# Optimization experiments

Hardware: AMD Instinct MI355X
Metric: run time of the kernel (lower is better)

Reference implementation:

```python
import jax, jax.numpy as jnp
import numpy as np

BETA = 1.0  # init kwarg beta
TAU = 0.5   # init kwarg tau


def setup_inputs() -> dict:
    key = jax.random.key(0)
    k1, k2, k3, k4, k5 = jax.random.split(key, 5)
    M, N, D = 6, 2048, 1152  # views, batch, flattened feature dim (Linear(1152,128))
    return {
        "x_all": jax.random.normal(k1, (M, N, D), jnp.float32),
        "W": jax.random.normal(k2, (D, 128), jnp.float32) * 0.03,  # line_layers weight (in,out)
        "b": jax.random.normal(k3, (128,), jnp.float32) * 0.01,    # line_layers bias
        "U": jax.random.normal(k4, (128, 64), jnp.float32),
        "V": jax.random.normal(k5, (128, 64), jnp.float32),
    }


def _retrieve(x, P):
    # x: [M, N, 128], P: [128, 64]
    # per-sample: P @ softmax(beta * (P.T @ x_i))  ==  softmax(beta * x @ P) @ P.T  (batched)
    attn = jax.nn.softmax(BETA * jnp.einsum('mnd,dk->mnk', x, P), axis=-1)  # [M,N,64]
    return jnp.einsum('mnk,dk->mnd', attn, P)  # [M,N,128]


def _pair_loss_sum(E):
    # E: [M, N, 128]. Sum of losses over all ordered pairs of distinct views.
    M, N = E.shape[0], E.shape[1]
    sim = jnp.einsum('mnd,kpd->mknp', E, E) / TAU          # [M,M,N,N]
    pos = jnp.diagonal(sim, axis1=2, axis2=3)              # [M,M,N] positives (diag)
    # negatives = off-diagonal entries of each row; exclude diag via -inf for stable logsumexp
    neg = jnp.where(jnp.eye(N, dtype=bool), -jnp.inf, sim)
    lse = jax.nn.logsumexp(neg, axis=-1)                   # [M,M,N]
    # -log(exp(pos)/sum(exp(neg))) == lse - pos
    per_pair = (lse - pos).mean(axis=-1)                   # [M,M]
    off_diag = 1.0 - jnp.eye(M, dtype=per_pair.dtype)      # skip i == j (torch.equal check)
    return (per_pair * off_diag).sum()


def reference(x_all, W, b, U, V):
    M, N = x_all.shape[0], x_all.shape[1]
    x = x_all.reshape(M, N, -1) @ W + b                    # Linear(1152, 128)
    Ue = _retrieve(x, U)
    Ve = _retrieve(x, V)
    total = _pair_loss_sum(Ue) + _pair_loss_sum(Ve)
    return total / (2 * M * (M - 1))
```

## Files before the change

kernel.cpp:

```cpp
#include <hip/hip_runtime.h>
#include <hip/hip_bf16.h>

#define M_VIEWS 6
#define N_ROWS  2048
#define D_IN    1152
#define D_HID   128
#define D_K     64
#define TOT_ROWS (M_VIEWS * N_ROWS)
#define SCALE_E 1.6986436f
#define LOG2E   1.4426950408889634f

typedef short bf16x8 __attribute__((ext_vector_type(8)));
typedef float f32x4  __attribute__((ext_vector_type(4)));

typedef __attribute__((address_space(1))) const void gvoid_t;
typedef __attribute__((address_space(3))) void svoid_t;

__device__ inline void async16(const void* g, void* l) {
    __builtin_amdgcn_global_load_lds((gvoid_t*)g, (svoid_t*)l, 16, 0, 0);
}

#if __has_builtin(__builtin_amdgcn_exp2f)
__device__ inline float fexp2(float x) { return __builtin_amdgcn_exp2f(x); }
#else
__device__ inline float fexp2(float x) { return exp2f(x); }
#endif
#if __has_builtin(__builtin_amdgcn_logf)
__device__ inline float flog2(float x) { return __builtin_amdgcn_logf(x); }
#else
__device__ inline float flog2(float x) { return log2f(x); }
#endif

__device__ inline short2 splitf(float v) {
    __hip_bfloat16 hb = __float2bfloat16(v);
    float rem = v - __bfloat162float(hb);
    __hip_bfloat16 lb = __float2bfloat16(rem);
    short2 r;
    r.x = *reinterpret_cast<const short*>(&hb);
    r.y = *reinterpret_cast<const short*>(&lb);
    return r;
}

__device__ inline short bf16of(float v) {
    __hip_bfloat16 hb = __float2bfloat16(v);
    return *reinterpret_cast<const short*>(&hb);
}

__global__ __launch_bounds__(64) void prep_w_kernel(
    const float* __restrict__ W, __hip_bfloat16* __restrict__ Whi)
{
    const int s    = blockIdx.x >> 3;
    const int ct   = blockIdx.x & 7;
    const int lane = threadIdx.x;
    const int lg = lane >> 4, lr = lane & 15;
    bf16x8 hi;
    #pragma unroll
    for (int i = 0; i < 8; ++i)
        hi[i] = bf16of(W[(size_t)(s * 32 + lg * 8 + i) * D_HID + ct * 16 + lr]);
    size_t off = ((size_t)(s * 8 + ct) * 64 + lane) * 8;
    *reinterpret_cast<bf16x8*>(Whi + off) = hi;
}

__global__ __launch_bounds__(64) void prep_p_kernel(
    const float* __restrict__ U, const float* __restrict__ V,
    __hip_bfloat16* __restrict__ Pfhi, __hip_bfloat16* __restrict__ Pflo)
{
    const int blk = blockIdx.x;
    const int mat = blk >> 5, f = blk & 31;
    const float* P = mat ? V : U;
    const int lane = threadIdx.x, lg = lane >> 4, lr = lane & 15;
    bf16x8 hi, lo;
    #pragma unroll
    for (int i = 0; i < 8; ++i) {
        float w;
        if (f < 16) {
            int s = f >> 2, ct = f & 3;
            w = P[(size_t)(s * 32 + lg * 8 + i) * D_K + ct * 16 + lr] * LOG2E;
        } else {
            int g = f - 16, s2 = g >> 3, ct2 = g & 7;
            w = P[(size_t)(ct2 * 16 + lr) * D_K + s2 * 32 + lg * 8 + i];
        }
        short2 hl = splitf(w);
        hi[i] = hl.x; lo[i] = hl.y;
    }
    size_t off = ((size_t)(mat * 32 + f) * 64 + lane) * 8;
    *reinterpret_cast<bf16x8*>(Pfhi + off) = hi;
    *reinterpret_cast<bf16x8*>(Pflo + off) = lo;
}

__global__ __launch_bounds__(256) void xretrieve_kernel(
    const float* __restrict__ xall,
    const __hip_bfloat16* __restrict__ Whi,
    const float* __restrict__ bias,
    const __hip_bfloat16* __restrict__ Pfhi,
    const __hip_bfloat16* __restrict__ Pflo,
    __hip_bfloat16* __restrict__ E)
{
    __shared__ __align__(16) char smem[24576];
    f32x4* red = reinterpret_cast<f32x4*>(smem);
    float* xs  = reinterpret_cast<float*>(smem);
    float* alb = reinterpret_cast<float*>(smem + 8448);

    const int wave = threadIdx.x >> 6, lane = threadIdx.x & 63;
    const int lg = lane >> 4, lr = lane & 15;
    const int row0 = blockIdx.x * 16;

    const float* ap = xall + (size_t)(row0 + lr) * D_IN + wave * 288;
    f32x4 acc[8];
    #pragma unroll
    for (int ct = 0; ct < 8; ++ct) acc[ct] = {0.f, 0.f, 0.f, 0.f};

    const bf16x8* whb = reinterpret_cast<const bf16x8*>(Whi) + lane;
    for (int s = 0; s < 9; ++s) {
        const int gs = wave * 9 + s;
        const float* a8 = ap + s * 32 + lg * 8;
        float4 va = *reinterpret_cast<const float4*>(a8);
        float4 vb = *reinterpret_cast<const float4*>(a8 + 4);
        bf16x8 ah;
        ah[0] = bf16of(va.x); ah[1] = bf16of(va.y);
        ah[2] = bf16of(va.z); ah[3] = bf16of(va.w);
        ah[4] = bf16of(vb.x); ah[5] = bf16of(vb.y);
        ah[6] = bf16of(vb.z); ah[7] = bf16of(vb.w);
        #pragma unroll
        for (int ct = 0; ct < 8; ++ct) {
            bf16x8 wh = whb[(size_t)(gs * 8 + ct) * 64];
            acc[ct] = __builtin_amdgcn_mfma_f32_16x16x32_bf16(ah, wh, acc[ct], 0, 0, 0);
        }
    }

    if (wave > 0) {
        #pragma unroll
        for (int ct = 0; ct < 8; ++ct)
            red[(wave - 1) * 512 + ct * 64 + lane] = acc[ct];
    }
    __syncthreads();
    if (wave == 0) {
        f32x4 xv[8];
        #pragma unroll
        for (int ct = 0; ct < 8; ++ct) {
            f32x4 a = acc[ct];
            a += red[ct * 64 + lane];
            a += red[512 + ct * 64 + lane];
            a += red[1024 + ct * 64 + lane];
            float bj = bias[ct * 16 + lr];
            #pragma unroll
            for (int j = 0; j < 4; ++j) xv[ct][j] = a[j] + bj;
        }
        __syncthreads();
        #pragma unroll
        for (int ct = 0; ct < 8; ++ct)
            #pragma unroll
            for (int j = 0; j < 4; ++j)
                xs[(lg * 4 + j) * 132 + ct * 16 + lr] = xv[ct][j];
    } else {
        __syncthreads();
    }
    __syncthreads();

    const int mat = wave;
    if (wave < 2) {
        bf16x8 xh[4], xl[4];
        #pragma unroll
        for (int s = 0; s < 4; ++s) {
            const float* xp = xs + lr * 132 + s * 32 + lg * 8;
            float4 va = *reinterpret_cast<const float4*>(xp);
            float4 vb = *reinterpret_cast<const float4*>(xp + 4);
            float v[8] = {va.x, va.y, va.z, va.w, vb.x, vb.y, vb.z, vb.w};
            #pragma unroll
            for (int i = 0; i < 8; ++i) {
                short2 hl = splitf(v[i]);
                xh[s][i] = hl.x; xl[s][i] = hl.y;
            }
        }

        const bf16x8* bh = reinterpret_cast<const bf16x8*>(Pfhi) + (size_t)mat * 32 * 64 + lane;
        const bf16x8* bl = reinterpret_cast<const bf16x8*>(Pflo) + (size_t)mat * 32 * 64 + lane;

        f32x4 lacc[4];
        #pragma unroll
        for (int ct = 0; ct < 4; ++ct) lacc[ct] = {0.f, 0.f, 0.f, 0.f};
        #pragma unroll
        for (int ct = 0; ct < 4; ++ct) {
            #pragma unroll
            for (int s = 0; s < 4; ++s) {
                bf16x8 wh = bh[(s * 4 + ct) * 64];
                bf16x8 wl = bl[(s * 4 + ct) * 64];
                lacc[ct] = __builtin_amdgcn_mfma_f32_16x16x32_bf16(xh[s], wh, lacc[ct], 0, 0, 0);
                lacc[ct] = __builtin_amdgcn_mfma_f32_16x16x32_bf16(xl[s], wh, lacc[ct], 0, 0, 0);
                lacc[ct] = __builtin_amdgcn_mfma_f32_16x16x32_bf16(xh[s], wl, lacc[ct], 0, 0, 0);
            }
        }

        float* al = alb + mat * (16 * 72);
        #pragma unroll
        for (int j = 0; j < 4; ++j) {
            float l0 = lacc[0][j], l1 = lacc[1][j], l2 = lacc[2][j], l3 = lacc[3][j];
            float mx = fmaxf(fmaxf(l0, l1), fmaxf(l2, l3));
            #pragma unroll
            for (int s = 1; s < 16; s <<= 1) mx = fmaxf(mx, __shfl_xor(mx, s));
            float p0 = fexp2(l0 - mx), p1 = fexp2(l1 - mx);
            float p2 = fexp2(l2 - mx), p3 = fexp2(l3 - mx);
            float sm = p0 + p1 + p2 + p3;
            #pragma unroll
            for (int s = 1; s < 16; s <<= 1) sm += __shfl_xor(sm, s);
            float inv = 1.0f / sm;
            float* ar = al + (lg * 4 + j) * 72;
            ar[lr]      = p0 * inv;
            ar[16 + lr] = p1 * inv;
            ar[32 + lr] = p2 * inv;
            ar[48 + lr] = p3 * inv;
        }
    }
    __syncthreads();

    if (wave < 2) {
        const float* al = alb + mat * (16 * 72);
        const bf16x8* bh = reinterpret_cast<const bf16x8*>(Pfhi) + (size_t)mat * 32 * 64 + lane;
        const bf16x8* bl = reinterpret_cast<const bf16x8*>(Pflo) + (size_t)mat * 32 * 64 + lane;

        bf16x8 aah[2], aal[2];
        #pragma unroll
        for (int s2 = 0; s2 < 2; ++s2) {
            const float* ap2 = al + lr * 72 + s2 * 32 + lg * 8;
            float4 va = *reinterpret_cast<const float4*>(ap2);
            float4 vb = *reinterpret_cast<const float4*>(ap2 + 4);
            float v[8] = {va.x, va.y, va.z, va.w, vb.x, vb.y, vb.z, vb.w};
            #pragma unroll
            for (int i = 0; i < 8; ++i) {
                short2 hl = splitf(v[i]);
                aah[s2][i] = hl.x; aal[s2][i] = hl.y;
            }
        }

        f32x4 eacc[8];
        #pragma unroll
        for (int ct2 = 0; ct2 < 8; ++ct2) eacc[ct2] = {0.f, 0.f, 0.f, 0.f};
        #pragma unroll
        for (int ct2 = 0; ct2 < 8; ++ct2) {
            #pragma unroll
            for (int s2 = 0; s2 < 2; ++s2) {
                bf16x8 wh = bh[(16 + s2 * 8 + ct2) * 64];
                bf16x8 wl = bl[(16 + s2 * 8 + ct2) * 64];
                eacc[ct2] = __builtin_amdgcn_mfma_f32_16x16x32_bf16(aah[s2], wh, eacc[ct2], 0, 0, 0);
                eacc[ct2] = __builtin_amdgcn_mfma_f32_16x16x32_bf16(aal[s2], wh, eacc[ct2], 0, 0, 0);
                eacc[ct2] = __builtin_amdgcn_mfma_f32_16x16x32_bf16(aah[s2], wl, eacc[ct2], 0, 0, 0);
            }
        }

        __hip_bfloat16* Er = E + ((size_t)mat * TOT_ROWS + row0) * D_HID;
        #pragma unroll
        for (int ct2 = 0; ct2 < 8; ++ct2) {
            #pragma unroll
            for (int j = 0; j < 4; ++j)
                Er[(size_t)(lg * 4 + j) * D_HID + ct2 * 16 + lr] =
                    __float2bfloat16(eacc[ct2][j] * SCALE_E);
        }
    }
}

__global__ __launch_bounds__(512) void pair_lse_kernel(
    const __hip_bfloat16* __restrict__ E,
    float* __restrict__ partial)
{
    __shared__ __align__(16) unsigned char kbuf[2 * 16384];

    const int bid    = blockIdx.x;
    const int linear = (bid & 7) * 120 + (bid >> 3);
    const int half = linear & 1;
    const int qt   = (linear >> 1) & 7;
    const int job  = linear >> 4;
    const int mat = job / 30;
    const int pr  = job % 30;
    const int m   = pr / 5;
    int k = pr % 5; k += (k >= m);

    const __hip_bfloat16* Qm = E + ((size_t)(mat * M_VIEWS + m)) * N_ROWS * D_HID;
    const __hip_bfloat16* Kk = E + ((size_t)(mat * M_VIEWS + k)) * N_ROWS * D_HID;

    const int tid  = threadIdx.x;
    const int wave = tid >> 6, lane = tid & 63;
    const int lr = lane & 15, lg = lane >> 4;

    const int qrow0 = qt * 256 + wave * 32;

    bf16x8 afrag[2][4];
    #pragma unroll
    for (int rf = 0; rf < 2; ++rf) {
        const __hip_bfloat16* qp = Qm + (size_t)(qrow0 + rf * 16 + lr) * D_HID;
        #pragma unroll
        for (int s = 0; s < 4; ++s)
            afrag[rf][s] = *reinterpret_cast<const bf16x8*>(qp + s * 32 + lg * 8);
    }

    float mrun[2][4], lrun[2][4], pos[2][4];
    #pragma unroll
    for (int rf = 0; rf < 2; ++rf)
        #pragma unroll
        for (int j = 0; j < 4; ++j) {
            mrun[rf][j] = -1e30f; lrun[rf][j] = 0.f; pos[rf][j] = 0.f;
        }

    const int ptdiag = qt * 4 + (wave >> 1);
    const int ctd0   = (wave & 1) * 2;
    const int pt0    = half * 16;

    #define STAGE(pt, b)                                                        \
        {                                                                       \
            const char* base = (const char*)Kk + (size_t)(pt) * 16384;          \
            _Pragma("unroll")                                                   \
            for (int i = 0; i < 2; ++i) {                                       \
                int f = wave * 2 + i;                                           \
                int ct_ = f >> 2, s_ = f & 3;                                   \
                async16(base + (ct_ * 16 + lr) * 256 + s_ * 64 + lg * 16,       \
                        kbuf + (b) * 16384 + f * 1024);                         \
            }                                                                   \
        }

    STAGE(pt0, 0);
    __syncthreads();

    const unsigned char* kb0 = kbuf + lane * 16;
    for (int t = 0; t < 16; ++t) {
        const int pt = pt0 + t;
        if (t < 15) STAGE(pt + 1, (t + 1) & 1);

        const unsigned char* kb = kb0 + (t & 1) * 16384;
        f32x4 acc[2][4];
        #pragma unroll
        for (int rf = 0; rf < 2; ++rf)
            #pragma unroll
            for (int ct = 0; ct < 4; ++ct) acc[rf][ct] = {0.f, 0.f, 0.f, 0.f};

        #pragma unroll
        for (int ct = 0; ct < 4; ++ct) {
            #pragma unroll
            for (int s = 0; s < 4; ++s) {
                bf16x8 bf = *reinterpret_cast<const bf16x8*>(kb + (ct * 4 + s) * 1024);
                acc[0][ct] = __builtin_amdgcn_mfma_f32_16x16x32_bf16(afrag[0][s], bf, acc[0][ct], 0, 0, 0);
                acc[1][ct] = __builtin_amdgcn_mfma_f32_16x16x32_bf16(afrag[1][s], bf, acc[1][ct], 0, 0, 0);
            }
        }

        const bool dtile = (pt == ptdiag);
        #pragma unroll
        for (int rf = 0; rf < 2; ++rf) {
            #pragma unroll
            for (int j = 0; j < 4; ++j) {
                float v0 = acc[rf][0][j], v1 = acc[rf][1][j];
                float v2 = acc[rf][2][j], v3 = acc[rf][3][j];
                if (dtile) {
                    const int cd = ctd0 + rf;
                    const bool dl = (lr == lg * 4 + j);
                    float vd = (cd == 0) ? v0 : (cd == 1) ? v1 : (cd == 2) ? v2 : v3;
                    if (dl) {
                        pos[rf][j] = vd;
                        float nv = -INFINITY;
                        if      (cd == 0) v0 = nv;
                        else if (cd == 1) v1 = nv;
                        else if (cd == 2) v2 = nv;
                        else              v3 = nv;
                    }
                }
                float tmax = fmaxf(fmaxf(v0, v1), fmaxf(v2, v3));
                float nm = fmaxf(mrun[rf][j], tmax);
                float ps = fexp2(v0 - nm) + fexp2(v1 - nm)
                         + fexp2(v2 - nm) + fexp2(v3 - nm);
                lrun[rf][j] = lrun[rf][j] * fexp2(mrun[rf][j] - nm) + ps;
                mrun[rf][j] = nm;
            }
        }
        __syncthreads();
    }

    #pragma unroll
    for (int rf = 0; rf < 2; ++rf) {
        #pragma unroll
        for (int j = 0; j < 4; ++j) {
            float Mv = mrun[rf][j], Lv = lrun[rf][j];
            #pragma unroll
            for (int s = 1; s < 16; s <<= 1) {
                float Mo = __shfl_xor(Mv, s);
                float Lo = __shfl_xor(Lv, s);
                float nm = fmaxf(Mv, Mo);
                Lv = Lv * fexp2(Mv - nm) + Lo * fexp2(Mo - nm);
                Mv = nm;
            }
            float P = pos[rf][j];
            #pragma unroll
            for (int s = 1; s < 16; s <<= 1) P += __shfl_xor(P, s);
            if (lr == 0) {
                const int row = qrow0 + rf * 16 + lg * 4 + j;
                float* dst = partial + (((size_t)job * N_ROWS + row) * 2 + half) * 3;
                dst[0] = Mv; dst[1] = Lv; dst[2] = P;
            }
        }
    }
}

__global__ __launch_bounds__(256) void merge_kernel(
    const float* __restrict__ partial, float* __restrict__ out, float scale)
{
    __shared__ float wsum[4];
    const int r = blockIdx.x * 256 + threadIdx.x;
    const float* p = partial + (size_t)r * 6;
    float m0 = p[0], l0 = p[1], p0 = p[2];
    float m1 = p[3], l1 = p[4], p1 = p[5];
    float ms = fmaxf(m0, m1);
    float L  = l0 * fexp2(m0 - ms) + l1 * fexp2(m1 - ms);
    float c  = (ms + flog2(L)) - (p0 + p1);

    #pragma unroll
    for (int s = 1; s < 64; s <<= 1) c += __shfl_xor(c, s);
    const int wave = threadIdx.x >> 6, lane = threadIdx.x & 63;
    if (lane == 0) wsum[wave] = c;
    __syncthreads();
    if (threadIdx.x == 0)
        atomicAdd(out, (wsum[0] + wsum[1] + wsum[2] + wsum[3]) * scale);
}

extern "C" void kernel_launch(void* const* d_in, const int* in_sizes, int n_in,
                              void* d_out, int out_size, void* d_ws, size_t ws_size,
                              hipStream_t stream) {
    const float* xall = (const float*)d_in[0];
    const float* W    = (const float*)d_in[1];
    const float* b    = (const float*)d_in[2];
    const float* U    = (const float*)d_in[3];
    const float* V    = (const float*)d_in[4];
    float* out = (float*)d_out;

    char* ws = (char*)d_ws;
    __hip_bfloat16* E   = (__hip_bfloat16*)ws;
    __hip_bfloat16* Whi = E + 2 * (size_t)TOT_ROWS * D_HID;
    __hip_bfloat16* Pfhi = Whi + 36 * 8 * 64 * 8;
    __hip_bfloat16* Pflo = Pfhi + 2 * 32 * 64 * 8;
    float* partial = (float*)(Pflo + 2 * 32 * 64 * 8);

    (void)hipMemsetAsync(d_out, 0, sizeof(float), stream);

    prep_w_kernel<<<36 * 8, 64, 0, stream>>>(W, Whi);
    prep_p_kernel<<<64, 64, 0, stream>>>(U, V, Pfhi, Pflo);
    xretrieve_kernel<<<TOT_ROWS / 16, 256, 0, stream>>>(xall, Whi, b, Pfhi, Pflo, E);

    pair_lse_kernel<<<960, 512, 0, stream>>>(E, partial);

    const float scale = 0.6931471805599453f / (2048.0f * 60.0f);
    merge_kernel<<<60 * 2048 / 256, 256, 0, stream>>>(partial, out, scale);
}
```

Measured before the change: 133.2 us.

## Widen xretrieve to 8 waves, split K and retrieval output across waves, merge prep kernels

The projection kernel moves from 4 to 8 waves per block. The K dimension is split 5/4 steps per wave, with a two-level LDS reduction, and the final retrieval GEMM is spread across all 8 waves (mat x column pairs) instead of 2. The two prep kernels are fused into one launch. The aim is more memory-level parallelism on the x stream and less serial tail work per block, at the cost of more LDS, extra barriers and possibly lower occupancy.

```diff
diff --git a/kernel.cpp b/kernel.cpp
--- a/kernel.cpp
+++ b/kernel.cpp
@@ -46,49 +46,49 @@
     return *reinterpret_cast<const short*>(&hb);
 }
 
-__global__ __launch_bounds__(64) void prep_w_kernel(
-    const float* __restrict__ W, __hip_bfloat16* __restrict__ Whi)
+__global__ __launch_bounds__(64) void prep_kernel(
+    const float* __restrict__ W,
+    const float* __restrict__ U, const float* __restrict__ V,
+    __hip_bfloat16* __restrict__ Whi,
+    __hip_bfloat16* __restrict__ Pfhi, __hip_bfloat16* __restrict__ Pflo)
 {
-    const int s    = blockIdx.x >> 3;
-    const int ct   = blockIdx.x & 7;
     const int lane = threadIdx.x;
     const int lg = lane >> 4, lr = lane & 15;
-    bf16x8 hi;
-    #pragma unroll
-    for (int i = 0; i < 8; ++i)
-        hi[i] = bf16of(W[(size_t)(s * 32 + lg * 8 + i) * D_HID + ct * 16 + lr]);
-    size_t off = ((size_t)(s * 8 + ct) * 64 + lane) * 8;
-    *reinterpret_cast<bf16x8*>(Whi + off) = hi;
-}
-
-__global__ __launch_bounds__(64) void prep_p_kernel(
-    const float* __restrict__ U, const float* __restrict__ V,
-    __hip_bfloat16* __restrict__ Pfhi, __hip_bfloat16* __restrict__ Pflo)
-{
-    const int blk = blockIdx.x;
-    const int mat = blk >> 5, f = blk & 31;
-    const float* P = mat ? V : U;
-    const int lane = threadIdx.x, lg = lane >> 4, lr = lane & 15;
-    bf16x8 hi, lo;
-    #pragma unroll
-    for (int i = 0; i < 8; ++i) {
-        float w;
-        if (f < 16) {
-            int s = f >> 2, ct = f & 3;
-            w = P[(size_t)(s * 32 + lg * 8 + i) * D_K + ct * 16 + lr] * LOG2E;
-        } else {
-            int g = f - 16, s2 = g >> 3, ct2 = g & 7;
-            w = P[(size_t)(ct2 * 16 + lr) * D_K + s2 * 32 + lg * 8 + i];
-        }
-        short2 hl = splitf(w);
-        hi[i] = hl.x; lo[i] = hl.y;
-    }
-    size_t off = ((size_t)(mat * 32 + f) * 64 + lane) * 8;
-    *reinterpret_cast<bf16x8*>(Pfhi + off) = hi;
-    *reinterpret_cast<bf16x8*>(Pflo + off) = lo;
-}
-
-__global__ __launch_bounds__(256) void xretrieve_kernel(
+
+    if (blockIdx.x < 288) {
+        const int s  = blockIdx.x >> 3;
+        const int ct = blockIdx.x & 7;
+        bf16x8 hi;
+        #pragma unroll
+        for (int i = 0; i < 8; ++i)
+            hi[i] = bf16of(W[(size_t)(s * 32 + lg * 8 + i) * D_HID + ct * 16 + lr]);
+        size_t off = ((size_t)(s * 8 + ct) * 64 + lane) * 8;
+        *reinterpret_cast<bf16x8*>(Whi + off) = hi;
+    } else {
+        const int blk = blockIdx.x - 288;
+        const int mat = blk >> 5, f = blk & 31;
+        const float* P = mat ? V : U;
+        bf16x8 hi, lo;
+        #pragma unroll
+        for (int i = 0; i < 8; ++i) {
+            float w;
+            if (f < 16) {
+                int s = f >> 2, ct = f & 3;
+                w = P[(size_t)(s * 32 + lg * 8 + i) * D_K + ct * 16 + lr] * LOG2E;
+            } else {
+                int g = f - 16, s2 = g >> 3, ct2 = g & 7;
+                w = P[(size_t)(ct2 * 16 + lr) * D_K + s2 * 32 + lg * 8 + i];
+            }
+            short2 hl = splitf(w);
+            hi[i] = hl.x; lo[i] = hl.y;
+        }
+        size_t off = ((size_t)(mat * 32 + f) * 64 + lane) * 8;
+        *reinterpret_cast<bf16x8*>(Pfhi + off) = hi;
+        *reinterpret_cast<bf16x8*>(Pflo + off) = lo;
+    }
+}
+
+__global__ __launch_bounds__(512) void xretrieve_kernel(
     const float* __restrict__ xall,
     const __hip_bfloat16* __restrict__ Whi,
     const float* __restrict__ bias,
@@ -96,23 +96,26 @@
     const __hip_bfloat16* __restrict__ Pflo,
     __hip_bfloat16* __restrict__ E)
 {
-    __shared__ __align__(16) char smem[24576];
+    __shared__ __align__(16) char smem[32768 + 8448 + 9216];
     f32x4* red = reinterpret_cast<f32x4*>(smem);
-    float* xs  = reinterpret_cast<float*>(smem);
-    float* alb = reinterpret_cast<float*>(smem + 8448);
+    float* xs  = reinterpret_cast<float*>(smem + 32768);
+    float* alb = reinterpret_cast<float*>(smem + 32768 + 8448);
 
     const int wave = threadIdx.x >> 6, lane = threadIdx.x & 63;
     const int lg = lane >> 4, lr = lane & 15;
     const int row0 = blockIdx.x * 16;
 
-    const float* ap = xall + (size_t)(row0 + lr) * D_IN + wave * 288;
+    const int nst = (wave < 4) ? 5 : 4;
+    const int st0 = (wave < 4) ? wave * 5 : 20 + (wave - 4) * 4;
+    const float* ap = xall + (size_t)(row0 + lr) * D_IN + st0 * 32;
+
     f32x4 acc[8];
     #pragma unroll
     for (int ct = 0; ct < 8; ++ct) acc[ct] = {0.f, 0.f, 0.f, 0.f};
 
     const bf16x8* whb = reinterpret_cast<const bf16x8*>(Whi) + lane;
-    for (int s = 0; s < 9; ++s) {
-        const int gs = wave * 9 + s;
+    for (int s = 0; s < nst; ++s) {
+        const int gs = st0 + s;
         const float* a8 = ap + s * 32 + lg * 8;
         float4 va = *reinterpret_cast<const float4*>(a8);
         float4 vb = *reinterpret_cast<const float4*>(a8 + 4);
@@ -128,14 +131,25 @@
         }
     }
 
-    if (wave > 0) {
+    if (wave >= 4) {
+        #pragma unroll
+        for (int ct = 0; ct < 8; ++ct)
+            red[(wave - 4) * 512 + ct * 64 + lane] = acc[ct];
+    }
+    __syncthreads();
+    if (wave < 4) {
+        #pragma unroll
+        for (int ct = 0; ct < 8; ++ct)
+            acc[ct] += red[wave * 512 + ct * 64 + lane];
+    }
+    __syncthreads();
+    if (wave >= 1 && wave < 4) {
         #pragma unroll
         for (int ct = 0; ct < 8; ++ct)
             red[(wave - 1) * 512 + ct * 64 + lane] = acc[ct];
     }
     __syncthreads();
     if (wave == 0) {
-        f32x4 xv[8];
         #pragma unroll
         for (int ct = 0; ct < 8; ++ct) {
             f32x4 a = acc[ct];
@@ -144,21 +158,14 @@
             a += red[1024 + ct * 64 + lane];
             float bj = bias[ct * 16 + lr];
             #pragma unroll
-            for (int j = 0; j < 4; ++j) xv[ct][j] = a[j] + bj;
-        }
-        __syncthreads();
-        #pragma unroll
-        for (int ct = 0; ct < 8; ++ct)
-            #pragma unroll
             for (int j = 0; j < 4; ++j)
-                xs[(lg * 4 + j) * 132 + ct * 16 + lr] = xv[ct][j];
-    } else {
-        __syncthreads();
-    }
-    __syncthreads();
-
-    const int mat = wave;
+                xs[(lg * 4 + j) * 132 + ct * 16 + lr] = a[j] + bj;
+        }
+    }
+    __syncthreads();
+
     if (wave < 2) {
+        const int mat = wave;
         bf16x8 xh[4], xl[4];
         #pragma unroll
         for (int s = 0; s < 4; ++s) {
@@ -213,10 +220,12 @@
     }
     __syncthreads();
 
-    if (wave < 2) {
-        const float* al = alb + mat * (16 * 72);
-        const bf16x8* bh = reinterpret_cast<const bf16x8*>(Pfhi) + (size_t)mat * 32 * 64 + lane;
-        const bf16x8* bl = reinterpret_cast<const bf16x8*>(Pflo) + (size_t)mat * 32 * 64 + lane;
+    {
+        const int mat2 = wave & 1;
+        const int cp   = wave >> 1;
+        const float* al = alb + mat2 * (16 * 72);
+        const bf16x8* bh = reinterpret_cast<const bf16x8*>(Pfhi) + (size_t)mat2 * 32 * 64 + lane;
+        const bf16x8* bl = reinterpret_cast<const bf16x8*>(Pflo) + (size_t)mat2 * 32 * 64 + lane;
 
         bf16x8 aah[2], aal[2];
         #pragma unroll
@@ -232,28 +241,23 @@
             }
         }
 
-        f32x4 eacc[8];
-        #pragma unroll
-        for (int ct2 = 0; ct2 < 8; ++ct2) eacc[ct2] = {0.f, 0.f, 0.f, 0.f};
-        #pragma unroll
-        for (int ct2 = 0; ct2 < 8; ++ct2) {
+        __hip_bfloat16* Er = E + ((size_t)mat2 * TOT_ROWS + row0) * D_HID;
+        #pragma unroll
+        for (int q = 0; q < 2; ++q) {
+            const int ct2 = cp * 2 + q;
+            f32x4 eacc = {0.f, 0.f, 0.f, 0.f};
             #pragma unroll
             for (int s2 = 0; s2 < 2; ++s2) {
                 bf16x8 wh = bh[(16 + s2 * 8 + ct2) * 64];
                 bf16x8 wl = bl[(16 + s2 * 8 + ct2) * 64];
-                eacc[ct2] = __builtin_amdgcn_mfma_f32_16x16x32_bf16(aah[s2], wh, eacc[ct2], 0, 0, 0);
-                eacc[ct2] = __builtin_amdgcn_mfma_f32_16x16x32_bf16(aal[s2], wh, eacc[ct2], 0, 0, 0);
-                eacc[ct2] = __builtin_amdgcn_mfma_f32_16x16x32_bf16(aah[s2], wl, eacc[ct2], 0, 0, 0);
-            }
-        }
-
-        __hip_bfloat16* Er = E + ((size_t)mat * TOT_ROWS + row0) * D_HID;
-        #pragma unroll
-        for (int ct2 = 0; ct2 < 8; ++ct2) {
+                eacc = __builtin_amdgcn_mfma_f32_16x16x32_bf16(aah[s2], wh, eacc, 0, 0, 0);
+                eacc = __builtin_amdgcn_mfma_f32_16x16x32_bf16(aal[s2], wh, eacc, 0, 0, 0);
+                eacc = __builtin_amdgcn_mfma_f32_16x16x32_bf16(aah[s2], wl, eacc, 0, 0, 0);
+            }
             #pragma unroll
             for (int j = 0; j < 4; ++j)
                 Er[(size_t)(lg * 4 + j) * D_HID + ct2 * 16 + lr] =
-                    __float2bfloat16(eacc[ct2][j] * SCALE_E);
+                    __float2bfloat16(eacc[j] * SCALE_E);
         }
     }
 }
@@ -437,9 +441,8 @@
 
     (void)hipMemsetAsync(d_out, 0, sizeof(float), stream);
 
-    prep_w_kernel<<<36 * 8, 64, 0, stream>>>(W, Whi);
-    prep_p_kernel<<<64, 64, 0, stream>>>(U, V, Pfhi, Pflo);
-    xretrieve_kernel<<<TOT_ROWS / 16, 256, 0, stream>>>(xall, Whi, b, Pfhi, Pflo, E);
+    prep_kernel<<<352, 64, 0, stream>>>(W, U, V, Whi, Pfhi, Pflo);
+    xretrieve_kernel<<<TOT_ROWS / 16, 512, 0, stream>>>(xall, Whi, b, Pfhi, Pflo, E);
 
     pair_lse_kernel<<<960, 512, 0, stream>>>(E, partial);
 
```

Result: no change. 134.4 us (+0.9%).
